# Kernel optimization log

Measured on AMD Instinct MI355X. Metric: run time of the kernel, lower is better.

## Reference

```python
import jax, jax.numpy as jnp
import numpy as np

N_NODES = 200000
D = 512
N_GRAPHS = 4096


def setup_inputs() -> dict:
    key = jax.random.key(0)
    k1, k2, k3 = jax.random.split(key, 3)
    V = jax.random.normal(k1, (N_NODES, D), dtype=jnp.float32)
    # nn.Linear(input_dim, 1): weight [1, d], bias [1]
    W = jax.random.normal(k2, (1, D), dtype=jnp.float32) / jnp.sqrt(jnp.float32(D))
    b_lin = jnp.zeros((1,), dtype=jnp.float32)
    batch_index = jnp.sort(jax.random.randint(k3, (N_NODES,), 0, N_GRAPHS, dtype=jnp.int32))
    return {"V": V, "W": W, "b_lin": b_lin, "batch_index": batch_index, "num_graphs": N_GRAPHS}


def reference(V, W, b_lin, batch_index, num_graphs):
    # scores = Linear(d_v, 1)(V)  -> [N]
    scores = V @ W[0] + b_lin[0]
    # scatter_softmax over segments (stable: subtract per-segment max)
    seg_max = jax.ops.segment_max(scores, batch_index, num_segments=num_graphs)
    e = jnp.exp(scores - seg_max[batch_index])
    denom = jax.ops.segment_sum(e, batch_index, num_segments=num_graphs)
    alpha = e / denom[batch_index]  # [N]
    # weighted scatter sum: H[g] = sum_{i in g} alpha_i * V_i  -> [b, d]
    H = jax.ops.segment_sum(alpha[:, None] * V, batch_index, num_segments=num_graphs)
    return H
```

## Files before the change

### kernel.cpp

```cpp
#include <hip/hip_runtime.h>
#include <math.h>


#define DIM 512
#define GR 4

typedef float vf4 __attribute__((ext_vector_type(4)));

__global__ __launch_bounds__(256)
void seg_bounds_scatter(const int* __restrict__ bi,
                        int* __restrict__ starts,
                        int n_nodes, int num_graphs)
{
    const int i = blockIdx.x * blockDim.x + threadIdx.x;
    if (i >= n_nodes) return;
    const int a = bi[i];
    if (i == 0) {
        for (int g = 0; g <= a; ++g) starts[g] = 0;
    }
    const int b = (i + 1 < n_nodes) ? bi[i + 1] : num_graphs;
    for (int g = a + 1; g <= b; ++g) starts[g] = i + 1;
}

__global__ __launch_bounds__(64, 4)
void gated_pool_wave(const float* __restrict__ V,
                     const float* __restrict__ W,
                     const float* __restrict__ b_lin,
                     const int* __restrict__ starts,
                     float* __restrict__ H)
{
    const int g    = blockIdx.x;
    const int lane = threadIdx.x;

    const int s = starts[g];
    const int e = starts[g + 1];

    float* outA = H + (size_t)g * DIM + lane * 4;
    float* outB = outA + 256;

    if (s >= e) {
        vf4 z = (vf4)(0.f);
        __builtin_nontemporal_store(z, (vf4*)outA);
        __builtin_nontemporal_store(z, (vf4*)outB);
        return;
    }

    const vf4 wA = *(const vf4*)(W + lane * 4);
    const vf4 wB = *(const vf4*)(W + 256 + lane * 4);
    const float bias = b_lin[0];

    const int len = e - s;
    const float* vbase = V + (size_t)s * DIM + lane * 4;

    float denom = 0.f;
    vf4   accA  = (vf4)(0.f);
    vf4   accB  = (vf4)(0.f);

    auto LOADF = [&](vf4 (&A)[GR], vf4 (&B)[GR], int gb) {
        #pragma unroll
        for (int r = 0; r < GR; ++r) {
            const vf4* p = (const vf4*)(vbase + (size_t)(gb + r) * DIM);
            A[r] = __builtin_nontemporal_load(p);
            B[r] = __builtin_nontemporal_load(p + 64);
        }
    };
    auto LOADT = [&](vf4 (&A)[GR], vf4 (&B)[GR], int gb, int nr) {
        #pragma unroll
        for (int r = 0; r < GR; ++r) {
            if (r < nr) {
                const vf4* p = (const vf4*)(vbase + (size_t)(gb + r) * DIM);
                A[r] = __builtin_nontemporal_load(p);
                B[r] = __builtin_nontemporal_load(p + 64);
            } else {
                A[r] = (vf4)(0.f);
                B[r] = (vf4)(0.f);
            }
        }
    };
    auto LOADG = [&](vf4 (&A)[GR], vf4 (&B)[GR], int gb) {
        if (gb + GR <= len) LOADF(A, B, gb);
        else                LOADT(A, B, gb, len - gb);
    };

    auto PROC = [&](vf4 (&A)[GR], vf4 (&B)[GR], int gb) {
        #pragma unroll
        for (int r = 0; r < GR; ++r) {
            const vf4 t = A[r] * wA + B[r] * wB;
            float p = t.x + t.y + t.z + t.w;
            #pragma unroll
            for (int off = 1; off < 64; off <<= 1)
                p += __shfl_xor(p, off, 64);
            const float er = (gb + r < len) ? __expf(p + bias) : 0.f;
            denom += er;
            accA  += er * A[r];
            accB  += er * B[r];
        }
    };

    vf4 a0[GR], b0[GR], a1[GR], b1[GR];
    LOADG(a0, b0, 0);
    int base = 0;
    while (true) {
        const bool more = (base + GR) < len;
        if (more) LOADG(a1, b1, base + GR);
        PROC(a0, b0, base);
        if (!more) break;
        const bool more2 = (base + 2 * GR) < len;
        if (more2) LOADG(a0, b0, base + 2 * GR);
        PROC(a1, b1, base + GR);
        if (!more2) break;
        base += 2 * GR;
    }

    const float inv = 1.f / denom;
    const vf4 oA = accA * inv;
    const vf4 oB = accB * inv;
    __builtin_nontemporal_store(oA, (vf4*)outA);
    __builtin_nontemporal_store(oB, (vf4*)outB);
}

extern "C" void kernel_launch(void* const* d_in, const int* in_sizes, int n_in,
                              void* d_out, int out_size, void* d_ws, size_t ws_size,
                              hipStream_t stream)
{
    const float* V     = (const float*)d_in[0];
    const float* W     = (const float*)d_in[1];
    const float* b_lin = (const float*)d_in[2];
    const int*   bidx  = (const int*)d_in[3];
    const int n_nodes    = in_sizes[3];
    const int num_graphs = out_size / DIM;

    int* starts = (int*)d_ws;

    const int nb = (n_nodes + 255) / 256;
    seg_bounds_scatter<<<nb, 256, 0, stream>>>(bidx, starts, n_nodes, num_graphs);
    gated_pool_wave<<<num_graphs, 64, 0, stream>>>(
        V, W, b_lin, starts, (float*)d_out);
}
```

Before: 77.61 us.

## Replace segment-bounds kernel with in-wave 64-ary binary search

Removes the separate scatter kernel that computed segment start offsets. Each wave now finds its segment start and end with a cooperative 64-way search over the sorted batch index, using ballot and shuffle. This saves one kernel launch and the trip of the starts array through global memory. In exchange every wave runs about three rounds of dependent gather loads before it starts streaming V.

Result: no change. 76.14 us (-1.9%).

```diff
diff --git a/kernel.cpp b/kernel.cpp
--- a/kernel.cpp
+++ b/kernel.cpp
@@ -7,33 +7,37 @@
 
 typedef float vf4 __attribute__((ext_vector_type(4)));
 
-__global__ __launch_bounds__(256)
-void seg_bounds_scatter(const int* __restrict__ bi,
-                        int* __restrict__ starts,
-                        int n_nodes, int num_graphs)
+__device__ __forceinline__
+int wave_lower_bound(const int* __restrict__ bi, int n, int target, int lane)
 {
-    const int i = blockIdx.x * blockDim.x + threadIdx.x;
-    if (i >= n_nodes) return;
-    const int a = bi[i];
-    if (i == 0) {
-        for (int g = 0; g <= a; ++g) starts[g] = 0;
+    int lo = 0, hi = n;
+    while (hi > lo) {
+        const int w = hi - lo;
+        const int p = lo + (int)(((long long)w * (lane + 1)) / 65);
+        const bool cond = bi[p] < target;
+        const unsigned long long mask = __ballot(cond);
+        const int c = __popcll(mask);
+        int nlo = lo, nhi = hi;
+        if (c > 0)  nlo = __shfl(p, c - 1, 64) + 1;
+        if (c < 64) nhi = __shfl(p, c, 64);
+        lo = nlo; hi = nhi;
     }
-    const int b = (i + 1 < n_nodes) ? bi[i + 1] : num_graphs;
-    for (int g = a + 1; g <= b; ++g) starts[g] = i + 1;
+    return lo;
 }
 
 __global__ __launch_bounds__(64, 4)
 void gated_pool_wave(const float* __restrict__ V,
                      const float* __restrict__ W,
                      const float* __restrict__ b_lin,
-                     const int* __restrict__ starts,
-                     float* __restrict__ H)
+                     const int* __restrict__ bi,
+                     float* __restrict__ H,
+                     int n_nodes)
 {
     const int g    = blockIdx.x;
     const int lane = threadIdx.x;
 
-    const int s = starts[g];
-    const int e = starts[g + 1];
+    const int s = wave_lower_bound(bi, n_nodes, g,     lane);
+    const int e = wave_lower_bound(bi, n_nodes, g + 1, lane);
 
     float* outA = H + (size_t)g * DIM + lane * 4;
     float* outB = outA + 256;
@@ -130,10 +134,6 @@
     const int n_nodes    = in_sizes[3];
     const int num_graphs = out_size / DIM;
 
-    int* starts = (int*)d_ws;
-
-    const int nb = (n_nodes + 255) / 256;
-    seg_bounds_scatter<<<nb, 256, 0, stream>>>(bidx, starts, n_nodes, num_graphs);
     gated_pool_wave<<<num_graphs, 64, 0, stream>>>(
-        V, W, b_lin, starts, (float*)d_out);
+        V, W, b_lin, bidx, (float*)d_out, n_nodes);
 }
```
